# Performance work log

Measured on AMD Instinct MI355X. Metric: run time of the kernel, lower is better.

The kernel has to match this reference:

```python
import jax, jax.numpy as jnp
import numpy as np

HIDDEN = 1024
SINK = 4
RECENT = 19  # int(window_size=64 * 0.3)
COMPRESSION_RATIO = 0.5


def setup_inputs() -> dict:
    key = jax.random.key(0)
    ks = jax.random.split(key, 10)
    B, S, H = 4, 4096, HIDDEN
    xav = lambda k, fi, fo: jax.random.normal(k, (fi, fo), jnp.float32) * np.sqrt(2.0 / (fi + fo))
    return {
        'keys': jax.random.normal(ks[0], (B, S, H), jnp.float32),
        'values': jax.random.normal(ks[1], (B, S, H), jnp.float32),
        # attention_predictor: Linear(H, H//2) -> ReLU -> Linear(H//2, 1) -> Sigmoid
        'W1a': xav(ks[2], H, H // 2), 'b1a': jnp.zeros((H // 2,), jnp.float32),
        'W2a': xav(ks[3], H // 2, 1), 'b2a': jnp.zeros((1,), jnp.float32),
        # importance_estimator: Linear(H, H//4) -> ReLU -> Linear(H//4, 1)
        'W1i': xav(ks[4], H, H // 4), 'b1i': jnp.zeros((H // 4,), jnp.float32),
        'W2i': xav(ks[5], H // 4, 1), 'b2i': jnp.zeros((1,), jnp.float32),
    }


def _token_scores(keys, values, W1a, b1a, W2a, b2a, W1i, b1i, W2i, b2i):
    att = jax.nn.sigmoid(jnp.einsum('bsh,ho->bso', jax.nn.relu(keys @ W1a + b1a), W2a) + b2a)[..., 0]
    imp = (jnp.einsum('bsh,ho->bso', jax.nn.relu(values @ W1i + b1i), W2i) + b2i)[..., 0]
    return 0.6 * att + 0.4 * imp  # [B, S]


def _selection_mask(scores):
    B, S = scores.shape
    keep_count = max(int(S * (1.0 - COMPRESSION_RATIO)), SINK + RECENT)
    mask = jnp.zeros((B, S), dtype=bool)
    mask = mask.at[:, :SINK].set(True)
    mask = mask.at[:, S - RECENT:].set(True)
    mid_len = S - RECENT - SINK
    if mid_len > 0:
        middle_keep = keep_count - SINK - RECENT
        if middle_keep > 0:
            k = min(middle_keep, mid_len)
            _, idx = jax.lax.top_k(scores[:, SINK:S - RECENT], k)  # [B, k]
            rows = jnp.arange(B)[:, None]
            mask = mask.at[rows, idx + SINK].set(True)
    return mask


def reference(keys, values, W1a, b1a, W2a, b2a, W1i, b1i, W2i, b2i):
    scores = _token_scores(keys, values, W1a, b1a, W2a, b2a, W1i, b1i, W2i, b2i)
    mask = _selection_mask(scores).astype(keys.dtype)[..., None]  # [B, S, 1]
    return keys * mask, values * mask
```

## Files before the change

### kernel.cpp

```cpp
#include <hip/hip_runtime.h>
#include <math.h>

#define H      1024
#define NA     512
#define NI     256
#define SEQ    4096
#define BATCH  4
#define NTOK   (BATCH*SEQ)
#define SINKN  4
#define RECENTN 19
#define MIDN   (SEQ - SINKN - RECENTN)
#define KSEL   2025
#define CHK    16

#define TT   128
#define UT   128
#define KC   32
#define ATT_BLOCKS ((NTOK/TT) * (NA/UT))
#define IMP_BLOCKS ((NTOK/TT) * (NI/UT))

__global__ __launch_bounds__(256, 2) void score_gemm_kernel(
    const float* __restrict__ keys, const float* __restrict__ values,
    const float* __restrict__ W1a, const float* __restrict__ b1a,
    const float* __restrict__ W2a,
    const float* __restrict__ W1i, const float* __restrict__ b1i,
    const float* __restrict__ W2i,
    float* __restrict__ part)
{
    __shared__ __align__(16) float smem[KC * 128 + KC * UT];
    float* A_lds = smem;
    float* B_lds = smem + KC * 128;

    const int tid = threadIdx.x;
    const int tx  = tid & 15;
    const int ty  = tid >> 4;
    const int bid = blockIdx.x;

    const bool is_att = bid < ATT_BLOCKS;
    const int  lb     = is_att ? bid : bid - ATT_BLOCKS;
    const int  tile   = is_att ? (lb >> 2) : (lb >> 1);
    const int  pass   = is_att ? (lb & 3)  : (lb & 1);
    const int  slot   = is_att ? pass : 4 + pass;
    const int  tokb   = tile * TT;
    const int  u0     = pass * UT;
    const int  wstride = is_att ? NA : NI;

    const float* Aptr = is_att ? keys : values;
    const float* Wptr = (is_att ? W1a : W1i) + u0;
    const float* b1p  = (is_att ? b1a : b1i) + u0;
    const float* w2p  = (is_att ? W2a : W2i) + u0;

    float acc[8][8];
#pragma unroll
    for (int t = 0; t < 8; ++t)
#pragma unroll
        for (int u = 0; u < 8; ++u) acc[t][u] = 0.f;

    const int at = tid >> 3;
    const int aq = tid & 7;
    const float* a_base = Aptr + (size_t)(tokb + at) * H + aq * 4;
    float* aw = A_lds + (aq * 4) * 128 + (at ^ ((aq & 3) << 3));

    const int bqi = tid & 31;
    const int rb  = tid >> 5;
    const float* b_base = Wptr + (size_t)rb * wstride + bqi * 4;
    float* bw = B_lds + rb * UT + ((bqi ^ (bqi >> 3)) << 2);
    const int q1 = 2 * tx, q2 = 2 * tx + 1;
    const int boff1 = ((q1 ^ (q1 >> 3)) << 2);
    const int boff2 = ((q2 ^ (q2 >> 3)) << 2);

    for (int h0 = 0; h0 < H; h0 += KC) {
        float4 aR[4], bR[4];
#pragma unroll
        for (int p = 0; p < 4; ++p)
            aR[p] = *(const float4*)(a_base + h0 + (size_t)p * 32 * H);
#pragma unroll
        for (int p = 0; p < 4; ++p)
            bR[p] = *(const float4*)(b_base + (size_t)(h0 + p * 8) * wstride);

        __syncthreads();
#pragma unroll
        for (int p = 0; p < 4; ++p) {
            aw[0 * 128 + p * 32] = aR[p].x;
            aw[1 * 128 + p * 32] = aR[p].y;
            aw[2 * 128 + p * 32] = aR[p].z;
            aw[3 * 128 + p * 32] = aR[p].w;
        }
#pragma unroll
        for (int p = 0; p < 4; ++p)
            *(float4*)&bw[p * 8 * UT] = bR[p];
        __syncthreads();

#pragma unroll 8
        for (int h = 0; h < KC; ++h) {
            const int tys = ((ty ^ ((h >> 2) & 3)) << 3);
            float a[8], b[8];
            *(float4*)&a[0] = *(const float4*)&A_lds[h * 128 + tys];
            *(float4*)&a[4] = *(const float4*)&A_lds[h * 128 + tys + 4];
            *(float4*)&b[0] = *(const float4*)&B_lds[h * UT + boff1];
            *(float4*)&b[4] = *(const float4*)&B_lds[h * UT + boff2];
#pragma unroll
            for (int t = 0; t < 8; ++t)
#pragma unroll
                for (int u = 0; u < 8; ++u)
                    acc[t][u] = fmaf(a[t], b[u], acc[t][u]);
        }
    }

    float b1v[8], w2v[8];
    *(float4*)&b1v[0] = *(const float4*)(b1p + tx * 8);
    *(float4*)&b1v[4] = *(const float4*)(b1p + tx * 8 + 4);
    *(float4*)&w2v[0] = *(const float4*)(w2p + tx * 8);
    *(float4*)&w2v[4] = *(const float4*)(w2p + tx * 8 + 4);

    __syncthreads();
    float* red = smem;
#pragma unroll
    for (int t = 0; t < 8; ++t) {
        float s = 0.f;
#pragma unroll
        for (int u = 0; u < 8; ++u)
            s += fmaxf(acc[t][u] + b1v[u], 0.f) * w2v[u];
        red[(ty * 8 + t) * 17 + tx] = s;
    }
    __syncthreads();
    if (tid < TT) {
        float s = 0.f;
        for (int x = 0; x < 16; ++x) s += red[tid * 17 + x];
        part[(size_t)slot * NTOK + tokb + tid] = s;
    }
}

__device__ __forceinline__ int block_sum(int val, int* red, int tid)
{
#pragma unroll
    for (int off = 32; off > 0; off >>= 1) val += __shfl_down(val, off);
    if ((tid & 63) == 0) red[tid >> 6] = val;
    __syncthreads();
    const int total = red[0] + red[1] + red[2] + red[3];
    __syncthreads();
    return total;
}

__global__ __launch_bounds__(256) void select_kernel(
    const float* __restrict__ part, const float* __restrict__ b2a,
    const float* __restrict__ b2i, float* __restrict__ mask)
{
    __shared__ unsigned int ks[MIDN];
    __shared__ int hist[256];
    __shared__ int red[4];
    __shared__ int scan_s[256];
    __shared__ unsigned int sh_pref;
    __shared__ int sh_r;

    const int tid = threadIdx.x;
    const int row = blockIdx.x;
    const float ba  = b2a[0];
    const float bi2 = b2i[0];

    for (int i = tid; i < MIDN; i += 256) {
        const int tok = row * SEQ + SINKN + i;
        float sa = ((part[tok] + part[NTOK + tok]) + part[2 * NTOK + tok]) + part[3 * NTOK + tok];
        float si = part[4 * NTOK + tok] + part[5 * NTOK + tok];
        const float att = 1.f / (1.f + expf(-(sa + ba)));
        const float s = 0.6f * att + 0.4f * (si + bi2);
        unsigned int u = __float_as_uint(s);
        u = (u & 0x80000000u) ? ~u : (u | 0x80000000u);
        ks[i] = u;
    }
    if (tid == 0) { sh_pref = 0u; sh_r = KSEL; }
    __syncthreads();

    for (int b = 3; b >= 0; --b) {
        hist[tid] = 0;
        __syncthreads();
        const unsigned int hi_mask = (b == 3) ? 0u : (0xFFFFFFFFu << ((b + 1) * 8));
        const unsigned int pref = sh_pref;
        for (int i = tid; i < MIDN; i += 256) {
            const unsigned int u = ks[i];
            if ((u & hi_mask) == pref)
                atomicAdd(&hist[(u >> (b * 8)) & 255], 1);
        }
        __syncthreads();

        scan_s[tid] = hist[tid];
        __syncthreads();
#pragma unroll
        for (int off = 1; off < 256; off <<= 1) {
            const int add = (tid + off < 256) ? scan_s[tid + off] : 0;
            __syncthreads();
            scan_s[tid] += add;
            __syncthreads();
        }
        const int r    = sh_r;
        const int sfx  = scan_s[tid];
        const int sfx1 = (tid < 255) ? scan_s[tid + 1] : 0;
        if (sfx >= r && sfx1 < r) {
            sh_r = r - sfx1;
            sh_pref = pref | ((unsigned int)tid << (b * 8));
        }
        __syncthreads();
    }
    const unsigned int v = sh_pref;

    const int st = tid * CHK;
    const int en = (st + CHK < MIDN) ? (st + CHK) : MIDN;

    int cgt = 0, ceq = 0;
    for (int k = st; k < en; ++k) { cgt += (ks[k] > v) ? 1 : 0; ceq += (ks[k] == v) ? 1 : 0; }
    const int total_gt = block_sum(cgt, red, tid);
    const int need = KSEL - total_gt;

    scan_s[tid] = ceq;
    __syncthreads();
#pragma unroll
    for (int off = 1; off < 256; off <<= 1) {
        const int add = (tid >= off) ? scan_s[tid - off] : 0;
        __syncthreads();
        scan_s[tid] += add;
        __syncthreads();
    }
    int r = scan_s[tid] - ceq;

    float* mr = mask + row * SEQ;
    for (int k = st; k < en; ++k) {
        const unsigned int u = ks[k];
        bool keep = false;
        if (u > v) keep = true;
        else if (u == v) { keep = (r < need); ++r; }
        mr[SINKN + k] = keep ? 1.f : 0.f;
    }
    for (int s = tid; s < SEQ; s += 256) {
        if (s < SINKN || s >= SEQ - RECENTN) mr[s] = 1.f;
    }
}

__global__ __launch_bounds__(256) void apply_kernel(
    const float* __restrict__ keys, const float* __restrict__ values,
    const float* __restrict__ mask, float* __restrict__ out)
{
    const int QT = NTOK * H / 4;
    const int stride = gridDim.x * 256;
    for (int i4 = blockIdx.x * 256 + threadIdx.x; i4 < 2 * QT; i4 += stride) {
        const bool isv = (i4 >= QT);
        const int  j4  = isv ? (i4 - QT) : i4;
        const float m  = mask[j4 >> 8];
        const float4* src = isv ? (const float4*)values : (const float4*)keys;
        const float4 x = src[j4];
        float4 y; y.x = x.x * m; y.y = x.y * m; y.z = x.z * m; y.w = x.w * m;
        ((float4*)out)[i4] = y;
    }
}

extern "C" void kernel_launch(void* const* d_in, const int* in_sizes, int n_in,
                              void* d_out, int out_size, void* d_ws, size_t ws_size,
                              hipStream_t stream)
{
    const float* keys   = (const float*)d_in[0];
    const float* values = (const float*)d_in[1];
    const float* W1a = (const float*)d_in[2];
    const float* b1a = (const float*)d_in[3];
    const float* W2a = (const float*)d_in[4];
    const float* b2a = (const float*)d_in[5];
    const float* W1i = (const float*)d_in[6];
    const float* b1i = (const float*)d_in[7];
    const float* W2i = (const float*)d_in[8];
    const float* b2i = (const float*)d_in[9];

    float* part = (float*)d_ws;
    float* mask = part + 6 * NTOK;

    score_gemm_kernel<<<ATT_BLOCKS + IMP_BLOCKS, 256, 0, stream>>>(
        keys, values, W1a, b1a, W2a, W1i, b1i, W2i, part);
    select_kernel<<<BATCH, 256, 0, stream>>>(part, b2a, b2i, mask);
    apply_kernel<<<8192, 256, 0, stream>>>(keys, values, mask, (float*)d_out);
}
```

Before: 568.5 us.

## Double-buffer weight tiles via direct global-to-LDS loads and remap thread tiling

The FP32 score GEMM now loads the weight tile straight into a double-buffered LDS region with global_load_lds, and prefetches the next activation chunk into registers after the barrier. This lets the next chunk's loads overlap the current chunk's FMAs and removes one barrier pair per iteration. The thread-to-output mapping changes to a per-wave 8x8 layout with new XOR swizzles meant to cut LDS bank conflicts. In exchange LDS use grows, which could lower occupancy, and the new swizzle and direct-to-LDS indexing must be exactly right.

```diff
diff --git a/kernel.cpp b/kernel.cpp
--- a/kernel.cpp
+++ b/kernel.cpp
@@ -16,8 +16,16 @@
 #define TT   128
 #define UT   128
 #define KC   32
+#define NCH  (H/KC)
 #define ATT_BLOCKS ((NTOK/TT) * (NA/UT))
 #define IMP_BLOCKS ((NTOK/TT) * (NI/UT))
+
+__device__ __forceinline__ void dma16(const float* g, float* l)
+{
+    __builtin_amdgcn_global_load_lds(
+        (const __attribute__((address_space(1))) void*)g,
+        (__attribute__((address_space(3))) void*)l, 16, 0, 0);
+}
 
 __global__ __launch_bounds__(256, 2) void score_gemm_kernel(
     const float* __restrict__ keys, const float* __restrict__ values,
@@ -27,13 +35,13 @@
     const float* __restrict__ W2i,
     float* __restrict__ part)
 {
-    __shared__ __align__(16) float smem[KC * 128 + KC * UT];
+    __shared__ __align__(16) float smem[KC * 128 + 2 * KC * 128];
     float* A_lds = smem;
-    float* B_lds = smem + KC * 128;
+    float* Bbuf  = smem + KC * 128;
 
     const int tid = threadIdx.x;
-    const int tx  = tid & 15;
-    const int ty  = tid >> 4;
+    const int lw  = tid & 63;
+    const int w   = tid >> 6;
     const int bid = blockIdx.x;
 
     const bool is_att = bid < ATT_BLOCKS;
@@ -50,55 +58,91 @@
     const float* b1p  = (is_att ? b1a : b1i) + u0;
     const float* w2p  = (is_att ? W2a : W2i) + u0;
 
-    float acc[8][8];
-#pragma unroll
-    for (int t = 0; t < 8; ++t)
-#pragma unroll
-        for (int u = 0; u < 8; ++u) acc[t][u] = 0.f;
+    const int T8 = (lw >> 3) | ((w & 1) << 3);
+    const int U8 = (lw & 7)  | ((w >> 1) << 3);
+
+    const int qA1 = 2 * T8,      qA2 = 2 * T8 + 1;
+    const int gA1 = qA1 ^ (qA1 >> 1);
+    const int gA2 = qA2 ^ (qA2 >> 1);
+    const int qB1 = 2 * U8,      qB2 = 2 * U8 + 1;
+    const int gB1 = (qB1 ^ (qB1 >> 1)) << 2;
+    const int gB2 = (qB2 ^ (qB2 >> 1)) << 2;
 
     const int at = tid >> 3;
     const int aq = tid & 7;
     const float* a_base = Aptr + (size_t)(tokb + at) * H + aq * 4;
-    float* aw = A_lds + (aq * 4) * 128 + (at ^ ((aq & 3) << 3));
-
-    const int bqi = tid & 31;
-    const int rb  = tid >> 5;
-    const float* b_base = Wptr + (size_t)rb * wstride + bqi * 4;
-    float* bw = B_lds + rb * UT + ((bqi ^ (bqi >> 3)) << 2);
-    const int q1 = 2 * tx, q2 = 2 * tx + 1;
-    const int boff1 = ((q1 ^ (q1 >> 3)) << 2);
-    const int boff2 = ((q2 ^ (q2 >> 3)) << 2);
-
-    for (int h0 = 0; h0 < H; h0 += KC) {
-        float4 aR[4], bR[4];
-#pragma unroll
-        for (int p = 0; p < 4; ++p)
-            aR[p] = *(const float4*)(a_base + h0 + (size_t)p * 32 * H);
-#pragma unroll
-        for (int p = 0; p < 4; ++p)
-            bR[p] = *(const float4*)(b_base + (size_t)(h0 + p * 8) * wstride);
-
-        __syncthreads();
-#pragma unroll
-        for (int p = 0; p < 4; ++p) {
-            aw[0 * 128 + p * 32] = aR[p].x;
-            aw[1 * 128 + p * 32] = aR[p].y;
-            aw[2 * 128 + p * 32] = aR[p].z;
-            aw[3 * 128 + p * 32] = aR[p].w;
-        }
-#pragma unroll
-        for (int p = 0; p < 4; ++p)
-            *(float4*)&bw[p * 8 * UT] = bR[p];
-        __syncthreads();
+    const int awb = (aq * 4) * 128 + (at & 3);
+    const int at4 = at >> 2;
+    const int q50 = at4,      q51 = at4 + 8, q52 = at4 + 16, q53 = at4 + 24;
+    const int of0 = (((q50 ^ (q50 >> 1)) ^ aq) << 2);
+    const int of1 = (((q51 ^ (q51 >> 1)) ^ aq) << 2);
+    const int of2 = (((q52 ^ (q52 >> 1)) ^ aq) << 2);
+    const int of3 = (((q53 ^ (q53 >> 1)) ^ aq) << 2);
+
+    const int sl   = lw & 31;
+    const int pisl = sl ^ (sl >> 1) ^ (sl >> 2) ^ (sl >> 3) ^ (sl >> 4);
+    const float* bg = Wptr + (size_t)(lw >> 5) * wstride + pisl * 4;
+    const int wrow = 8 * w;
+
+    float acc[8][8];
+#pragma unroll
+    for (int t = 0; t < 8; ++t)
+#pragma unroll
+        for (int u = 0; u < 8; ++u) acc[t][u] = 0.f;
+
+    float4 aR0 = *(const float4*)(a_base);
+    float4 aR1 = *(const float4*)(a_base + (size_t)32 * H);
+    float4 aR2 = *(const float4*)(a_base + (size_t)64 * H);
+    float4 aR3 = *(const float4*)(a_base + (size_t)96 * H);
+    dma16(bg + (size_t)(wrow + 0) * wstride, Bbuf + (wrow + 0) * 128);
+    dma16(bg + (size_t)(wrow + 2) * wstride, Bbuf + (wrow + 2) * 128);
+    dma16(bg + (size_t)(wrow + 4) * wstride, Bbuf + (wrow + 4) * 128);
+    dma16(bg + (size_t)(wrow + 6) * wstride, Bbuf + (wrow + 6) * 128);
+
+    for (int i = 0; i < NCH; ++i) {
+        float* Bcur = Bbuf + (i & 1) * (KC * 128);
+        float* Bnxt = Bbuf + ((i + 1) & 1) * (KC * 128);
+
+        __syncthreads();
+        A_lds[awb + 0 * 128 + of0] = aR0.x;
+        A_lds[awb + 1 * 128 + of0] = aR0.y;
+        A_lds[awb + 2 * 128 + of0] = aR0.z;
+        A_lds[awb + 3 * 128 + of0] = aR0.w;
+        A_lds[awb + 0 * 128 + of1] = aR1.x;
+        A_lds[awb + 1 * 128 + of1] = aR1.y;
+        A_lds[awb + 2 * 128 + of1] = aR1.z;
+        A_lds[awb + 3 * 128 + of1] = aR1.w;
+        A_lds[awb + 0 * 128 + of2] = aR2.x;
+        A_lds[awb + 1 * 128 + of2] = aR2.y;
+        A_lds[awb + 2 * 128 + of2] = aR2.z;
+        A_lds[awb + 3 * 128 + of2] = aR2.w;
+        A_lds[awb + 0 * 128 + of3] = aR3.x;
+        A_lds[awb + 1 * 128 + of3] = aR3.y;
+        A_lds[awb + 2 * 128 + of3] = aR3.z;
+        A_lds[awb + 3 * 128 + of3] = aR3.w;
+        __syncthreads();
+
+        if (i + 1 < NCH) {
+            const int hn = (i + 1) * KC;
+            aR0 = *(const float4*)(a_base + hn);
+            aR1 = *(const float4*)(a_base + hn + (size_t)32 * H);
+            aR2 = *(const float4*)(a_base + hn + (size_t)64 * H);
+            aR3 = *(const float4*)(a_base + hn + (size_t)96 * H);
+            const float* bgn = bg + (size_t)hn * wstride;
+            dma16(bgn + (size_t)(wrow + 0) * wstride, Bnxt + (wrow + 0) * 128);
+            dma16(bgn + (size_t)(wrow + 2) * wstride, Bnxt + (wrow + 2) * 128);
+            dma16(bgn + (size_t)(wrow + 4) * wstride, Bnxt + (wrow + 4) * 128);
+            dma16(bgn + (size_t)(wrow + 6) * wstride, Bnxt + (wrow + 6) * 128);
+        }
 
 #pragma unroll 8
         for (int h = 0; h < KC; ++h) {
-            const int tys = ((ty ^ ((h >> 2) & 3)) << 3);
+            const int rho = h >> 2;
             float a[8], b[8];
-            *(float4*)&a[0] = *(const float4*)&A_lds[h * 128 + tys];
-            *(float4*)&a[4] = *(const float4*)&A_lds[h * 128 + tys + 4];
-            *(float4*)&b[0] = *(const float4*)&B_lds[h * UT + boff1];
-            *(float4*)&b[4] = *(const float4*)&B_lds[h * UT + boff2];
+            *(float4*)&a[0] = *(const float4*)&A_lds[h * 128 + ((gA1 ^ rho) << 2)];
+            *(float4*)&a[4] = *(const float4*)&A_lds[h * 128 + ((gA2 ^ rho) << 2)];
+            *(float4*)&b[0] = *(const float4*)&Bcur[h * 128 + gB1];
+            *(float4*)&b[4] = *(const float4*)&Bcur[h * 128 + gB2];
 #pragma unroll
             for (int t = 0; t < 8; ++t)
 #pragma unroll
@@ -108,10 +152,10 @@
     }
 
     float b1v[8], w2v[8];
-    *(float4*)&b1v[0] = *(const float4*)(b1p + tx * 8);
-    *(float4*)&b1v[4] = *(const float4*)(b1p + tx * 8 + 4);
-    *(float4*)&w2v[0] = *(const float4*)(w2p + tx * 8);
-    *(float4*)&w2v[4] = *(const float4*)(w2p + tx * 8 + 4);
+    *(float4*)&b1v[0] = *(const float4*)(b1p + U8 * 8);
+    *(float4*)&b1v[4] = *(const float4*)(b1p + U8 * 8 + 4);
+    *(float4*)&w2v[0] = *(const float4*)(w2p + U8 * 8);
+    *(float4*)&w2v[4] = *(const float4*)(w2p + U8 * 8 + 4);
 
     __syncthreads();
     float* red = smem;
@@ -121,7 +165,7 @@
 #pragma unroll
         for (int u = 0; u < 8; ++u)
             s += fmaxf(acc[t][u] + b1v[u], 0.f) * w2v[u];
-        red[(ty * 8 + t) * 17 + tx] = s;
+        red[(T8 * 8 + t) * 17 + U8] = s;
     }
     __syncthreads();
     if (tid < TT) {
```

New measurement: 542.5 us. 1.05x faster.

## Restructure score GEMM with 8x16 register tiles and double-buffered async weight loads

Applied to the files above, without the earlier changes.

The scoring GEMM now runs 128-thread blocks, each thread holding an 8x16 accumulator tile, with a K-chunk of 16. Weight tiles are copied straight into a double-buffered LDS region via global_load_lds, and the next A chunk is prefetched into registers while the current chunk is computed. The aim is to hide global load latency and raise FMA work per LDS read, at the cost of higher register pressure (128 accumulators) and fewer threads per block.

```diff
diff --git a/kernel.cpp b/kernel.cpp
--- a/kernel.cpp
+++ b/kernel.cpp
@@ -15,11 +15,19 @@
 
 #define TT   128
 #define UT   128
-#define KC   32
-#define ATT_BLOCKS ((NTOK/TT) * (NA/UT))
-#define IMP_BLOCKS ((NTOK/TT) * (NI/UT))
-
-__global__ __launch_bounds__(256, 2) void score_gemm_kernel(
+#define KC   16
+#define NCH  (H/KC)
+#define ATT_BLOCKS 512
+#define IMP_BLOCKS 256
+
+__device__ __forceinline__ void dma16(const float* g, float* l)
+{
+    __builtin_amdgcn_global_load_lds(
+        (const __attribute__((address_space(1))) void*)g,
+        (__attribute__((address_space(3))) void*)l, 16, 0, 0);
+}
+
+__global__ __launch_bounds__(128, 2) void score_gemm_kernel(
     const float* __restrict__ keys, const float* __restrict__ values,
     const float* __restrict__ W1a, const float* __restrict__ b1a,
     const float* __restrict__ W2a,
@@ -27,107 +35,149 @@
     const float* __restrict__ W2i,
     float* __restrict__ part)
 {
-    __shared__ __align__(16) float smem[KC * 128 + KC * UT];
+    __shared__ __align__(16) float smem[KC * 128 + 2 * KC * 128];
     float* A_lds = smem;
-    float* B_lds = smem + KC * 128;
+    float* Bbuf  = smem + KC * 128;
 
     const int tid = threadIdx.x;
-    const int tx  = tid & 15;
-    const int ty  = tid >> 4;
+    const int lw  = tid & 63;
+    const int w   = tid >> 6;
     const int bid = blockIdx.x;
 
     const bool is_att = bid < ATT_BLOCKS;
     const int  lb     = is_att ? bid : bid - ATT_BLOCKS;
     const int  tile   = is_att ? (lb >> 2) : (lb >> 1);
-    const int  pass   = is_att ? (lb & 3)  : (lb & 1);
-    const int  slot   = is_att ? pass : 4 + pass;
+    const int  upass  = is_att ? (lb & 3)  : (lb & 1);
+    const int  slot   = is_att ? upass : 4 + upass;
     const int  tokb   = tile * TT;
-    const int  u0     = pass * UT;
+    const int  u0     = upass * UT;
     const int  wstride = is_att ? NA : NI;
 
-    const float* Aptr = is_att ? keys : values;
-    const float* Wptr = (is_att ? W1a : W1i) + u0;
-    const float* b1p  = (is_att ? b1a : b1i) + u0;
-    const float* w2p  = (is_att ? W2a : W2i) + u0;
-
-    float acc[8][8];
+    const float* Aptr  = is_att ? keys : values;
+    const float* Wbase = (is_att ? W1a : W1i) + u0;
+    const float* b1p   = (is_att ? b1a : b1i) + u0;
+    const float* w2p   = (is_att ? W2a : W2i) + u0;
+
+    const int T8  = tid >> 3;
+    const int U16 = tid & 7;
+
+    const int q0 = 4 * U16, q1 = q0 + 1, q2 = q0 + 2, q3 = q0 + 3;
+    const int bof0 = (q0 ^ (q0 >> 3)) << 2;
+    const int bof1 = (q1 ^ (q1 >> 3)) << 2;
+    const int bof2 = (q2 ^ (q2 >> 3)) << 2;
+    const int bof3 = (q3 ^ (q3 >> 3)) << 2;
+
+    const int at0 = tid >> 2;
+    const int aq  = tid & 3;
+    const float* aS = Aptr + (size_t)(tokb + at0) * H + aq * 4;
+    const int awb = (aq * 4) * 128 + ((((at0 >> 2) ^ (aq << 1))) << 2) + (at0 & 3);
+
+    const int sq   = lw & 31;
+    const int sigq = sq ^ (sq >> 3);
+    const float* bS = Wbase + (size_t)(2 * w + (lw >> 5)) * wstride + sigq * 4;
+    const int brow = 2 * w;
+
+    float acc[8][16];
 #pragma unroll
     for (int t = 0; t < 8; ++t)
 #pragma unroll
-        for (int u = 0; u < 8; ++u) acc[t][u] = 0.f;
-
-    const int at = tid >> 3;
-    const int aq = tid & 7;
-    const float* a_base = Aptr + (size_t)(tokb + at) * H + aq * 4;
-    float* aw = A_lds + (aq * 4) * 128 + (at ^ ((aq & 3) << 3));
-
-    const int bqi = tid & 31;
-    const int rb  = tid >> 5;
-    const float* b_base = Wptr + (size_t)rb * wstride + bqi * 4;
-    float* bw = B_lds + rb * UT + ((bqi ^ (bqi >> 3)) << 2);
-    const int q1 = 2 * tx, q2 = 2 * tx + 1;
-    const int boff1 = ((q1 ^ (q1 >> 3)) << 2);
-    const int boff2 = ((q2 ^ (q2 >> 3)) << 2);
-
-    for (int h0 = 0; h0 < H; h0 += KC) {
-        float4 aR[4], bR[4];
-#pragma unroll
-        for (int p = 0; p < 4; ++p)
-            aR[p] = *(const float4*)(a_base + h0 + (size_t)p * 32 * H);
-#pragma unroll
-        for (int p = 0; p < 4; ++p)
-            bR[p] = *(const float4*)(b_base + (size_t)(h0 + p * 8) * wstride);
-
-        __syncthreads();
-#pragma unroll
-        for (int p = 0; p < 4; ++p) {
-            aw[0 * 128 + p * 32] = aR[p].x;
-            aw[1 * 128 + p * 32] = aR[p].y;
-            aw[2 * 128 + p * 32] = aR[p].z;
-            aw[3 * 128 + p * 32] = aR[p].w;
-        }
-#pragma unroll
-        for (int p = 0; p < 4; ++p)
-            *(float4*)&bw[p * 8 * UT] = bR[p];
-        __syncthreads();
-
-#pragma unroll 8
+        for (int u = 0; u < 16; ++u) acc[t][u] = 0.f;
+
+    float4 aL0 = *(const float4*)(aS);
+    float4 aL1 = *(const float4*)(aS + (size_t)32 * H);
+    float4 aL2 = *(const float4*)(aS + (size_t)64 * H);
+    float4 aL3 = *(const float4*)(aS + (size_t)96 * H);
+    dma16(bS + (size_t) 0 * wstride, Bbuf + (brow +  0) * 128);
+    dma16(bS + (size_t) 4 * wstride, Bbuf + (brow +  4) * 128);
+    dma16(bS + (size_t) 8 * wstride, Bbuf + (brow +  8) * 128);
+    dma16(bS + (size_t)12 * wstride, Bbuf + (brow + 12) * 128);
+
+    for (int c = 0; c < NCH; ++c) {
+        float* Bcur = Bbuf + (c & 1) * (KC * 128);
+        float* Bnxt = Bbuf + ((c + 1) & 1) * (KC * 128);
+
+        __syncthreads();
+        A_lds[awb +  0 + 0 * 128] = aL0.x;
+        A_lds[awb +  0 + 1 * 128] = aL0.y;
+        A_lds[awb +  0 + 2 * 128] = aL0.z;
+        A_lds[awb +  0 + 3 * 128] = aL0.w;
+        A_lds[awb + 32 + 0 * 128] = aL1.x;
+        A_lds[awb + 32 + 1 * 128] = aL1.y;
+        A_lds[awb + 32 + 2 * 128] = aL1.z;
+        A_lds[awb + 32 + 3 * 128] = aL1.w;
+        A_lds[awb + 64 + 0 * 128] = aL2.x;
+        A_lds[awb + 64 + 1 * 128] = aL2.y;
+        A_lds[awb + 64 + 2 * 128] = aL2.z;
+        A_lds[awb + 64 + 3 * 128] = aL2.w;
+        A_lds[awb + 96 + 0 * 128] = aL3.x;
+        A_lds[awb + 96 + 1 * 128] = aL3.y;
+        A_lds[awb + 96 + 2 * 128] = aL3.z;
+        A_lds[awb + 96 + 3 * 128] = aL3.w;
+        __syncthreads();
+
+        if (c + 1 < NCH) {
+            const int hn = (c + 1) * KC;
+            aL0 = *(const float4*)(aS + hn);
+            aL1 = *(const float4*)(aS + hn + (size_t)32 * H);
+            aL2 = *(const float4*)(aS + hn + (size_t)64 * H);
+            aL3 = *(const float4*)(aS + hn + (size_t)96 * H);
+            const float* bgn = bS + (size_t)hn * wstride;
+            dma16(bgn + (size_t) 0 * wstride, Bnxt + (brow +  0) * 128);
+            dma16(bgn + (size_t) 4 * wstride, Bnxt + (brow +  4) * 128);
+            dma16(bgn + (size_t) 8 * wstride, Bnxt + (brow +  8) * 128);
+            dma16(bgn + (size_t)12 * wstride, Bnxt + (brow + 12) * 128);
+        }
+
+#pragma unroll
         for (int h = 0; h < KC; ++h) {
-            const int tys = ((ty ^ ((h >> 2) & 3)) << 3);
+            const int rho = (h >> 2) & 3;
+            const int ofa = h * 128 + (((2 * T8) ^ (rho << 1)) << 2);
             float a[8], b[8];
-            *(float4*)&a[0] = *(const float4*)&A_lds[h * 128 + tys];
-            *(float4*)&a[4] = *(const float4*)&A_lds[h * 128 + tys + 4];
-            *(float4*)&b[0] = *(const float4*)&B_lds[h * UT + boff1];
-            *(float4*)&b[4] = *(const float4*)&B_lds[h * UT + boff2];
+            *(float4*)&a[0] = *(const float4*)&A_lds[ofa];
+            *(float4*)&a[4] = *(const float4*)&A_lds[ofa + 4];
+            *(float4*)&b[0] = *(const float4*)&Bcur[h * 128 + bof0];
+            *(float4*)&b[4] = *(const float4*)&Bcur[h * 128 + bof1];
 #pragma unroll
             for (int t = 0; t < 8; ++t)
 #pragma unroll
                 for (int u = 0; u < 8; ++u)
                     acc[t][u] = fmaf(a[t], b[u], acc[t][u]);
-        }
-    }
-
-    float b1v[8], w2v[8];
-    *(float4*)&b1v[0] = *(const float4*)(b1p + tx * 8);
-    *(float4*)&b1v[4] = *(const float4*)(b1p + tx * 8 + 4);
-    *(float4*)&w2v[0] = *(const float4*)(w2p + tx * 8);
-    *(float4*)&w2v[4] = *(const float4*)(w2p + tx * 8 + 4);
+            *(float4*)&b[0] = *(const float4*)&Bcur[h * 128 + bof2];
+            *(float4*)&b[4] = *(const float4*)&Bcur[h * 128 + bof3];
+#pragma unroll
+            for (int t = 0; t < 8; ++t)
+#pragma unroll
+                for (int u = 0; u < 8; ++u)
+                    acc[t][8 + u] = fmaf(a[t], b[u], acc[t][8 + u]);
+        }
+    }
+
+    float s[8];
+#pragma unroll
+    for (int t = 0; t < 8; ++t) s[t] = 0.f;
+#pragma unroll
+    for (int qu = 0; qu < 4; ++qu) {
+        const float4 b1q = *(const float4*)(b1p + U16 * 16 + qu * 4);
+        const float4 w2q = *(const float4*)(w2p + U16 * 16 + qu * 4);
+#pragma unroll
+        for (int t = 0; t < 8; ++t) {
+            s[t] += fmaxf(acc[t][qu * 4 + 0] + b1q.x, 0.f) * w2q.x;
+            s[t] += fmaxf(acc[t][qu * 4 + 1] + b1q.y, 0.f) * w2q.y;
+            s[t] += fmaxf(acc[t][qu * 4 + 2] + b1q.z, 0.f) * w2q.z;
+            s[t] += fmaxf(acc[t][qu * 4 + 3] + b1q.w, 0.f) * w2q.w;
+        }
+    }
 
     __syncthreads();
     float* red = smem;
 #pragma unroll
-    for (int t = 0; t < 8; ++t) {
-        float s = 0.f;
-#pragma unroll
-        for (int u = 0; u < 8; ++u)
-            s += fmaxf(acc[t][u] + b1v[u], 0.f) * w2v[u];
-        red[(ty * 8 + t) * 17 + tx] = s;
-    }
+    for (int t = 0; t < 8; ++t)
+        red[(T8 * 8 + t) * 9 + U16] = s[t];
     __syncthreads();
     if (tid < TT) {
-        float s = 0.f;
-        for (int x = 0; x < 16; ++x) s += red[tid * 17 + x];
-        part[(size_t)slot * NTOK + tokb + tid] = s;
+        float sv = 0.f;
+        for (int x = 0; x < 8; ++x) sv += red[tid * 9 + x];
+        part[(size_t)slot * NTOK + tokb + tid] = sv;
     }
 }
 
@@ -270,7 +320,7 @@
     float* part = (float*)d_ws;
     float* mask = part + 6 * NTOK;
 
-    score_gemm_kernel<<<ATT_BLOCKS + IMP_BLOCKS, 256, 0, stream>>>(
+    score_gemm_kernel<<<ATT_BLOCKS + IMP_BLOCKS, 128, 0, stream>>>(
         keys, values, W1a, b1a, W2a, W1i, b1i, W2i, part);
     select_kernel<<<BATCH, 256, 0, stream>>>(part, b2a, b2i, mask);
     apply_kernel<<<8192, 256, 0, stream>>>(keys, values, mask, (float*)d_out);
```

Measured after the change: 1.130 ms. 98.7% more time.
